# Performance work log

Measured on AMD Instinct MI355X. Metric: run time of the kernel, lower is better.

Reference implementation:

```python
import jax, jax.numpy as jnp
import numpy as np

B_, L, HID = 2, 1024, 2048
N, H, P, NA = 128, 64, 64, 32   # state, heads, head_dim, rope angle pairs
DIN = 2 * H * P + 2 * N + 3 * H + NA  # 8672
EPS = 1e-5
A_FLOOR = 1e-4


def setup_inputs() -> dict:
    key = jax.random.key(0)
    k0, k1, k2 = jax.random.split(key, 3)
    hidden_states = jax.random.normal(k0, (B_, L, HID), jnp.float32)
    in_proj_w = jax.random.normal(k1, (DIN, HID), jnp.float32) * 0.02
    out_proj_w = jax.random.normal(k2, (HID, H * P), jnp.float32) * 0.02
    # dt_bias init exactly as in the torch module
    rng = np.random.default_rng(0)
    dt = np.exp(rng.random(H) * (np.log(0.1) - np.log(0.001)) + np.log(0.001))
    dt = np.clip(dt, 1e-4, None)
    dt_bias = jnp.asarray(dt + np.log(-np.expm1(-dt)), jnp.float32)
    return {
        'hidden_states': hidden_states,
        'in_proj_w': in_proj_w,
        'dt_bias': dt_bias,
        'B_bias': jnp.ones((H, N), jnp.float32),
        'C_bias': jnp.ones((H, N), jnp.float32),
        'B_norm_w': jnp.ones((N,), jnp.float32),
        'C_norm_w': jnp.ones((N,), jnp.float32),
        'D': jnp.ones((H,), jnp.float32),
        'out_proj_w': out_proj_w,
    }


def _rmsnorm(x, w):
    var = jnp.mean(jnp.square(x), axis=-1, keepdims=True)
    return x * jax.lax.rsqrt(var + EPS) * w


def _forward(hidden_states, in_proj_w, dt_bias, B_bias, C_bias,
             B_norm_w, C_norm_w, D, out_proj_w):
    b, l, _ = hidden_states.shape
    proj = hidden_states @ in_proj_w.T  # (b,l,DIN)
    splits = np.cumsum([H * P, H * P, N, N, H, H, H])
    z, x, Braw, Craw, dd_dt, dd_A, trap, angles = jnp.split(proj, splits, axis=-1)
    z = z.reshape(b, l, H, P)
    x = x.reshape(b, l, H, P)
    # data-dependent A (per token, per head), clamped
    A = jnp.minimum(-jax.nn.softplus(dd_A.astype(jnp.float32)), -A_FLOOR)
    DT = jax.nn.softplus(dd_dt + dt_bias)          # (b,l,H)
    decay = jnp.exp(A * DT)                        # (b,l,H)
    lam = jax.nn.sigmoid(trap)                     # trapezoidal weight (b,l,H)
    # RMSNorm then per-head input-independent bias (n_groups=1, mimo_rank=1)
    Bn = _rmsnorm(Braw, B_norm_w)[:, :, None, :] + B_bias  # (b,l,H,N)
    Cn = _rmsnorm(Craw, C_norm_w)[:, :, None, :] + C_bias  # (b,l,H,N)
    # blockwise rotary on first 2*NA state dims, cumulative data-dependent phase
    phase = jnp.cumsum(angles[:, :, None, :].astype(jnp.float32) * DT[..., None], axis=1)  # (b,l,H,NA)
    cos, sin = jnp.cos(phase), jnp.sin(phase)

    def rope(v):
        v1, v2, rest = v[..., :NA], v[..., NA:2 * NA], v[..., 2 * NA:]
        return jnp.concatenate([v1 * cos - v2 * sin, v1 * sin + v2 * cos, rest], axis=-1)

    Bh = rope(Bn.astype(jnp.float32))
    Ch = rope(Cn.astype(jnp.float32))
    u = (x * DT[..., None]).astype(jnp.float32)    # (b,l,H,P)

    # selective scan with generalized trapezoidal discretization:
    # h_t = a_t h_{t-1} + (1-lam_t) u_t B_t^T + lam_t a_t u_{t-1} B_{t-1}^T
    def step(carry, inp):
        h, Gp = carry
        Bt, Ct, ut, dec, lm = inp
        G = ut[..., :, None] * Bt[..., None, :]    # (b,H,P,N)
        h = dec[..., None, None] * h + (1.0 - lm)[..., None, None] * G \
            + (lm * dec)[..., None, None] * Gp
        y = jnp.einsum('bhpn,bhn->bhp', h, Ct)
        return (h, G), y

    h0 = jnp.zeros((b, H, P, N), jnp.float32)
    xs = (Bh.transpose(1, 0, 2, 3), Ch.transpose(1, 0, 2, 3),
          u.transpose(1, 0, 2, 3), decay.transpose(1, 0, 2), lam.transpose(1, 0, 2))
    _, ys = jax.lax.scan(step, (h0, h0), xs)       # (l,b,H,P)
    y = ys.transpose(1, 0, 2, 3)
    y = y + D[None, None, :, None] * x             # skip connection
    y = y * jax.nn.silu(z)                         # output gate (Z path in kernel)
    y = y.reshape(b, l, H * P)
    return y @ out_proj_w.T


def reference(hidden_states, in_proj_w, dt_bias, B_bias, C_bias,
              B_norm_w, C_norm_w, D, out_proj_w):
    return _forward(hidden_states, in_proj_w, dt_bias, B_bias, C_bias,
                    B_norm_w, C_norm_w, D, out_proj_w)
```

## Files before the change

### kernel.cpp

```cpp
#include <hip/hip_runtime.h>
#include <hip/hip_bf16.h>
#include <cstdint>
#include <cstddef>

#define DEVINL __device__ __forceinline__

typedef __attribute__((ext_vector_type(8))) short bf16x8;
typedef __attribute__((ext_vector_type(4))) float f32x4;

DEVINL float bf2f(unsigned short u){
  union { unsigned u32; float f; } cv; cv.u32 = ((unsigned)u) << 16; return cv.f;
}
DEVINL unsigned short f2bf(float f){
  union { float f; unsigned u32; } cv; cv.f = f;
  unsigned u = cv.u32;
  return (unsigned short)((u + 0x7FFFu + ((u >> 16) & 1u)) >> 16);
}
DEVINL float softplusf(float x){ return x > 20.f ? x : log1pf(expf(x)); }

DEVINL void g2l16(const void* gptr, void* ldsptr){
  __builtin_amdgcn_global_load_lds(
      (const __attribute__((address_space(1))) unsigned int*)gptr,
      (__attribute__((address_space(3))) unsigned int*)(uintptr_t)ldsptr,
      16, 0, 0);
}

DEVINL int swzb(int row, int col){ return row*256 + ((col*2) ^ ((row&7)<<4)); }
DEVINL void ldsw_write8(unsigned short* b, int row, int col, bf16x8 v){
  *(bf16x8*)((char*)b + swzb(row,col)) = v;
}
DEVINL bf16x8 ldsw_read8(const unsigned short* b, int row, int col){
  return *(const bf16x8*)((const char*)b + swzb(row,col));
}
DEVINL void ldsw_write1(unsigned short* b, int row, int col, unsigned short v){
  *(unsigned short*)((char*)b + swzb(row,col)) = v;
}
DEVINL unsigned short ldsw_read1(const unsigned short* b, int row, int col){
  return *(const unsigned short*)((const char*)b + swzb(row,col));
}

__global__ __launch_bounds__(256) void k_f32_to_bf16(
    const float* __restrict__ in, unsigned short* __restrict__ out, long n)
{
  long i = ((long)blockIdx.x * 256 + threadIdx.x) * 4;
  if (i + 3 < n){
    float4 v = *(const float4*)(in + i);
    unsigned long long pk =
        (unsigned long long)f2bf(v.x)
      | ((unsigned long long)f2bf(v.y) << 16)
      | ((unsigned long long)f2bf(v.z) << 32)
      | ((unsigned long long)f2bf(v.w) << 48);
    *(unsigned long long*)(out + i) = pk;
  }
}

template<bool OUT_BF16>
__global__ __launch_bounds__(256) void k_gemm_bt(
    const unsigned short* __restrict__ A,
    const unsigned short* __restrict__ Bt,
    void* __restrict__ Cout,
    int K, int Nrows, int Npad, int tiles_n)
{
  __shared__ unsigned short Asub[128*64];
  __shared__ unsigned short Bsub[128*64];
  const int tid = threadIdx.x;
  const int nwg = gridDim.x;
  const int wg = ((nwg & 7) == 0) ? (int)((blockIdx.x & 7) * (nwg >> 3) + (blockIdx.x >> 3))
                                  : (int)blockIdx.x;
  const int rt = wg / tiles_n, ct = wg % tiles_n;
  const int lane = tid & 63, wave = tid >> 6;
  const int wr = wave >> 1, wc = wave & 1;
  const int fr = lane & 15;
  const int fq = lane >> 4;

  const int srow0 = tid >> 3;
  const int sgrp  = (tid & 7) ^ ((tid >> 3) & 7);
  size_t aoff[4], boff[4];
  #pragma unroll
  for (int i = 0; i < 4; i++){
    int row = i*32 + srow0;
    aoff[i] = (size_t)(rt*128 + row) * K + sgrp*8;
    int brow = ct*128 + row; if (brow > Nrows-1) brow = Nrows-1;
    boff[i] = (size_t)brow * K + sgrp*8;
  }

  f32x4 acc[4][4] = {};

  for (int k0 = 0; k0 < K; k0 += 64){
    #pragma unroll
    for (int i = 0; i < 4; i++){
      g2l16(A  + aoff[i] + k0, (char*)Asub + (i*256 + tid)*16);
      g2l16(Bt + boff[i] + k0, (char*)Bsub + (i*256 + tid)*16);
    }
    asm volatile("s_waitcnt vmcnt(0)" ::: "memory");
    __syncthreads();

    #pragma unroll
    for (int kk = 0; kk < 2; kk++){
      bf16x8 af[4], bfr[4];
      const int slot = (kk*4 + fq) ^ (fr & 7);
      #pragma unroll
      for (int i = 0; i < 4; i++){
        int ra = wr*64 + i*16 + fr;
        int rb = wc*64 + i*16 + fr;
        af[i]  = *(const bf16x8*)((const char*)Asub + ra*128 + slot*16);
        bfr[i] = *(const bf16x8*)((const char*)Bsub + rb*128 + slot*16);
      }
      #pragma unroll
      for (int mi = 0; mi < 4; mi++)
        #pragma unroll
        for (int ni = 0; ni < 4; ni++)
          acc[mi][ni] = __builtin_amdgcn_mfma_f32_16x16x32_bf16(af[mi], bfr[ni], acc[mi][ni], 0, 0, 0);
    }
    __syncthreads();
  }

  const int er = (lane >> 4) * 4;
  const int ec = lane & 15;
  #pragma unroll
  for (int mi = 0; mi < 4; mi++){
    #pragma unroll
    for (int ni = 0; ni < 4; ni++){
      const int row = rt*128 + wr*64 + mi*16 + er;
      const int col = ct*128 + wc*64 + ni*16 + ec;
      #pragma unroll
      for (int r = 0; r < 4; r++){
        if (OUT_BF16)
          ((unsigned short*)Cout)[(size_t)(row+r)*Npad + col] = f2bf(acc[mi][ni][r]);
        else
          ((float*)Cout)[(size_t)(row+r)*Npad + col] = acc[mi][ni][r];
      }
    }
  }
}

__global__ __launch_bounds__(256) void k_prep_scalars(
    const unsigned short* __restrict__ proj, const float* __restrict__ dt_bias,
    float* __restrict__ DTt, float* __restrict__ logdec, float* __restrict__ lamt)
{
  int idx = blockIdx.x*256 + threadIdx.x;
  int h = idx & 63, row = idx >> 6;
  int b = row >> 10, l = row & 1023;
  size_t base = (size_t)row * 8704;
  float dd_dt = bf2f(proj[base + 8448 + h]);
  float dd_A  = bf2f(proj[base + 8512 + h]);
  float trap  = bf2f(proj[base + 8576 + h]);
  float DT = softplusf(dd_dt + dt_bias[h]);
  float A  = -fmaxf(softplusf(dd_A), 1e-4f);
  size_t o = ((size_t)(b*64 + h))*1024 + l;
  DTt[o]    = DT;
  logdec[o] = A * DT;
  lamt[o]   = 1.f / (1.f + expf(-trap));
}

__global__ __launch_bounds__(128) void k_rmsnorm(
    const unsigned short* __restrict__ proj, const float* __restrict__ Bw,
    const float* __restrict__ Cw, unsigned short* __restrict__ Bb2,
    unsigned short* __restrict__ Cb2)
{
  int row = blockIdx.x, n = threadIdx.x;
  size_t base = (size_t)row * 8704;
  float bv = bf2f(proj[base + 8192 + n]);
  float cv = bf2f(proj[base + 8320 + n]);
  float sb = bv*bv, sc = cv*cv;
  #pragma unroll
  for (int m = 1; m < 64; m <<= 1){ sb += __shfl_xor(sb, m, 64); sc += __shfl_xor(sc, m, 64); }
  __shared__ float red[4];
  if ((n & 63) == 0){ red[(n>>6)*2] = sb; red[(n>>6)*2+1] = sc; }
  __syncthreads();
  sb = red[0] + red[2];
  sc = red[1] + red[3];
  float rb = rsqrtf(sb*(1.f/128.f) + 1e-5f);
  float rc = rsqrtf(sc*(1.f/128.f) + 1e-5f);
  Bb2[row*128 + n] = f2bf(bv*rb*Bw[n]);
  Cb2[row*128 + n] = f2bf(cv*rc*Cw[n]);
}

__global__ __launch_bounds__(256) void k_chunkscan(
    const float* __restrict__ logdec, const float* __restrict__ lamt,
    float* __restrict__ clcb, float* __restrict__ gb)
{
  int bh = blockIdx.x;
  size_t base = (size_t)bh * 1024;
  int tid = threadIdx.x;
  int e0 = tid * 4;
  float v0 = logdec[base+e0], v1 = logdec[base+e0+1], v2 = logdec[base+e0+2], v3 = logdec[base+e0+3];
  float p0 = v0, p1 = p0+v1, p2 = p1+v2, p3 = p2+v3;
  float tot = p3;
  int sub = tid & 31;
  float incl = tot;
  #pragma unroll
  for (int off = 1; off < 32; off <<= 1){
    float u = __shfl_up(incl, off, 32);
    if (sub >= off) incl += u;
  }
  float excl = incl - tot;
  clcb[base+e0]   = excl + p0;
  clcb[base+e0+1] = excl + p1;
  clcb[base+e0+2] = excl + p2;
  clcb[base+e0+3] = excl + p3;
  #pragma unroll
  for (int i = 0; i < 4; i++){
    int l = e0 + i;
    int ln = (l == 1023) ? 1023 : l + 1;
    gb[base+l] = 1.f - lamt[base+l] + lamt[base+ln];
  }
}

__global__ __launch_bounds__(256) void k_phase(
    const unsigned short* __restrict__ proj, const float* __restrict__ DTt,
    unsigned short* __restrict__ cosb, unsigned short* __restrict__ sinb)
{
  int bh = blockIdx.x, b = bh >> 6, h = bh & 63;
  int na = threadIdx.x & 31, c = threadIdx.x >> 5;
  __shared__ float part[8][32];
  const float* dtr = DTt + (size_t)bh * 1024;
  float s = 0.f;
  for (int i = 0; i < 128; i++){
    int l = c*128 + i; int row = b*1024 + l;
    float ang = bf2f(proj[(size_t)row*8704 + 8640 + na]);
    s = fmaf(ang, dtr[l], s);
  }
  part[c][na] = s;
  __syncthreads();
  float off = 0.f;
  for (int cc = 0; cc < c; cc++) off += part[cc][na];
  float ph = off;
  for (int i = 0; i < 128; i++){
    int l = c*128 + i; int row = b*1024 + l;
    float ang = bf2f(proj[(size_t)row*8704 + 8640 + na]);
    ph = fmaf(ang, dtr[l], ph);
    float sn, cs;
    __sincosf(ph, &sn, &cs);
    size_t o = ((size_t)row*64 + h)*32 + na;
    cosb[o] = f2bf(cs); sinb[o] = f2bf(sn);
  }
}

__global__ __launch_bounds__(256, 1) void k_intra(
    const unsigned short* __restrict__ proj,
    const unsigned short* __restrict__ Bb2, const unsigned short* __restrict__ Cb2,
    const float* __restrict__ Bbias, const float* __restrict__ Cbias,
    const unsigned short* __restrict__ cosb, const unsigned short* __restrict__ sinb,
    const float* __restrict__ DTt, const float* __restrict__ clcb,
    const float* __restrict__ gb, const float* __restrict__ lamt,
    const float* __restrict__ Dv, unsigned short* __restrict__ ybf,
    unsigned short* __restrict__ Gbuf)
{
  const int c = blockIdx.x & 7, bh = blockIdx.x >> 3;
  const int b = bh >> 6, h = bh & 63;
  const int tid = threadIdx.x, lane = tid & 63, wave = tid >> 6;
  const int wr = wave >> 1, wc = wave & 1;
  const int fr = lane & 15, fq = lane >> 4;

  __shared__ __align__(16) unsigned short Cs[128*128];
  __shared__ __align__(16) unsigned short Bs[128*128];
  __shared__ __align__(16) unsigned short BTs[128*128];
  __shared__ __align__(16) unsigned short Uts[64*128];
  __shared__ float clcs[128], lams[128], gs[128], wUs[128], dts[128];
  __shared__ float biasB[128], biasC[128];

  const int base = b*1024 + c*128;
  const size_t shbase = (size_t)bh * 1024;
  const float Dh = Dv[h];

  if (tid < 128){
    int l = c*128 + tid;
    clcs[tid] = clcb[shbase + l];
    dts[tid]  = DTt[shbase + l];
    lams[tid] = lamt[shbase + l];
    gs[tid]   = gb[shbase + l];
    biasB[tid] = Bbias[h*128 + tid];
  } else {
    biasC[tid-128] = Cbias[h*128 + tid-128];
  }
  __syncthreads();
  if (tid < 128) wUs[tid] = __expf(clcs[127] - clcs[tid]) * gs[tid];

  {
    const int t = tid >> 1, half = tid & 1;
    const int grow = base + t;
    const size_t roff = (size_t)grow*128 + half*64;
    if (half == 0){
      bf16x8 cc[4], sv[4];
      #pragma unroll
      for (int i = 0; i < 4; i++){
        cc[i] = *(const bf16x8*)(cosb + ((size_t)grow*64 + h)*32 + i*8);
        sv[i] = *(const bf16x8*)(sinb + ((size_t)grow*64 + h)*32 + i*8);
      }
      #pragma unroll
      for (int i = 0; i < 4; i++){
        bf16x8 vlo = *(const bf16x8*)(Cb2 + roff + i*8);
        bf16x8 vhi = *(const bf16x8*)(Cb2 + roff + 32 + i*8);
        bf16x8 olo, ohi;
        #pragma unroll
        for (int e = 0; e < 8; e++){
          float a = bf2f((unsigned short)vlo[e]) + biasC[i*8+e];
          float d = bf2f((unsigned short)vhi[e]) + biasC[32+i*8+e];
          float cf = bf2f((unsigned short)cc[i][e]);
          float sf = bf2f((unsigned short)sv[i][e]);
          olo[e] = (short)f2bf(a*cf - d*sf);
          ohi[e] = (short)f2bf(a*sf + d*cf);
        }
        ldsw_write8(Cs, t, i*8, olo);
        ldsw_write8(Cs, t, 32 + i*8, ohi);
      }
      #pragma unroll
      for (int i = 0; i < 4; i++){
        bf16x8 vlo = *(const bf16x8*)(Bb2 + roff + i*8);
        bf16x8 vhi = *(const bf16x8*)(Bb2 + roff + 32 + i*8);
        bf16x8 olo, ohi;
        #pragma unroll
        for (int e = 0; e < 8; e++){
          float a = bf2f((unsigned short)vlo[e]) + biasB[i*8+e];
          float d = bf2f((unsigned short)vhi[e]) + biasB[32+i*8+e];
          float cf = bf2f((unsigned short)cc[i][e]);
          float sf = bf2f((unsigned short)sv[i][e]);
          olo[e] = (short)f2bf(a*cf - d*sf);
          ohi[e] = (short)f2bf(a*sf + d*cf);
        }
        ldsw_write8(Bs, t, i*8, olo);
        ldsw_write8(Bs, t, 32 + i*8, ohi);
        #pragma unroll
        for (int e = 0; e < 8; e++){
          ldsw_write1(BTs, i*8+e, t, (unsigned short)olo[e]);
          ldsw_write1(BTs, 32+i*8+e, t, (unsigned short)ohi[e]);
        }
      }
    } else {
      #pragma unroll
      for (int i = 0; i < 8; i++){
        bf16x8 v = *(const bf16x8*)(Cb2 + roff + i*8);
        bf16x8 o;
        #pragma unroll
        for (int e = 0; e < 8; e++) o[e] = (short)f2bf(bf2f((unsigned short)v[e]) + biasC[64+i*8+e]);
        ldsw_write8(Cs, t, 64 + i*8, o);
      }
      #pragma unroll
      for (int i = 0; i < 8; i++){
        bf16x8 v = *(const bf16x8*)(Bb2 + roff + i*8);
        bf16x8 o;
        #pragma unroll
        for (int e = 0; e < 8; e++) o[e] = (short)f2bf(bf2f((unsigned short)v[e]) + biasB[64+i*8+e]);
        ldsw_write8(Bs, t, 64 + i*8, o);
        #pragma unroll
        for (int e = 0; e < 8; e++) ldsw_write1(BTs, 64+i*8+e, t, (unsigned short)o[e]);
      }
    }
  }
  {
    const int p = tid & 63, jg = tid >> 6;
    #pragma unroll 4
    for (int i = 0; i < 32; i++){
      int j = jg*32 + i;
      size_t pb = (size_t)(base + j) * 8704;
      float x  = bf2f(proj[pb + 4096 + h*64 + p]);
      ldsw_write1(Uts, p, j, f2bf(x * dts[j]));
    }
  }
  __syncthreads();

  f32x4 acc1[4][4];
  #pragma unroll
  for (int mi = 0; mi < 4; mi++)
    #pragma unroll
    for (int ni = 0; ni < 4; ni++)
      acc1[mi][ni] = (f32x4){0.f,0.f,0.f,0.f};
  #pragma unroll
  for (int ks = 0; ks < 4; ks++){
    bf16x8 af[4], bj[4];
    #pragma unroll
    for (int mi = 0; mi < 4; mi++) af[mi] = ldsw_read8(Cs, wr*64+mi*16+fr, ks*32+fq*8);
    #pragma unroll
    for (int ni = 0; ni < 4; ni++) bj[ni] = ldsw_read8(Bs, wc*64+ni*16+fr, ks*32+fq*8);
    #pragma unroll
    for (int mi = 0; mi < 4; mi++)
      #pragma unroll
      for (int ni = 0; ni < 4; ni++)
        acc1[mi][ni] = __builtin_amdgcn_mfma_f32_16x16x32_bf16(af[mi], bj[ni], acc1[mi][ni], 0,0,0);
  }
  unsigned short pr[4][4][4];
  int jj[4]; float clcj[4], gj[4];
  #pragma unroll
  for (int ni = 0; ni < 4; ni++){ jj[ni] = wc*64+ni*16+fr; clcj[ni] = clcs[jj[ni]]; gj[ni] = gs[jj[ni]]; }
  #pragma unroll
  for (int mi = 0; mi < 4; mi++){
    #pragma unroll
    for (int r = 0; r < 4; r++){
      int t = wr*64+mi*16+fq*4+r;
      float ct = clcs[t], lt = lams[t];
      #pragma unroll
      for (int ni = 0; ni < 4; ni++){
        int j = jj[ni];
        float w = (j < t) ? __expf(ct - clcj[ni])*gj[ni] : ((j == t) ? (1.f - lt) : 0.f);
        pr[mi][ni][r] = f2bf(acc1[mi][ni][r] * w);
      }
    }
  }
  __syncthreads();
  #pragma unroll
  for (int mi = 0; mi < 4; mi++)
    #pragma unroll
    for (int ni = 0; ni < 4; ni++)
      #pragma unroll
      for (int r = 0; r < 4; r++)
        ldsw_write1(Bs, wr*64+mi*16+fq*4+r, wc*64+ni*16+fr, pr[mi][ni][r]);
  __syncthreads();

  f32x4 acc2[4][2];
  #pragma unroll
  for (int mi = 0; mi < 4; mi++)
    #pragma unroll
    for (int ni = 0; ni < 2; ni++)
      acc2[mi][ni] = (f32x4){0.f,0.f,0.f,0.f};
  #pragma unroll
  for (int ks = 0; ks < 4; ks++){
    bf16x8 af[4], uj[2];
    #pragma unroll
    for (int mi = 0; mi < 4; mi++) af[mi] = ldsw_read8(Bs, wr*64+mi*16+fr, ks*32+fq*8);
    #pragma unroll
    for (int ni = 0; ni < 2; ni++) uj[ni] = ldsw_read8(Uts, wc*32+ni*16+fr, ks*32+fq*8);
    #pragma unroll
    for (int mi = 0; mi < 4; mi++)
      #pragma unroll
      for (int ni = 0; ni < 2; ni++)
        acc2[mi][ni] = __builtin_amdgcn_mfma_f32_16x16x32_bf16(af[mi], uj[ni], acc2[mi][ni], 0,0,0);
  }
  f32x4 accS[2][4];
  #pragma unroll
  for (int mi = 0; mi < 2; mi++)
    #pragma unroll
    for (int ni = 0; ni < 4; ni++)
      accS[mi][ni] = (f32x4){0.f,0.f,0.f,0.f};
  #pragma unroll
  for (int ks = 0; ks < 4; ks++){
    bf16x8 au[2], bn[4];
    #pragma unroll
    for (int mi = 0; mi < 2; mi++){
      bf16x8 raw = ldsw_read8(Uts, wr*32+mi*16+fr, ks*32+fq*8);
      #pragma unroll
      for (int e = 0; e < 8; e++){
        float f = bf2f((unsigned short)raw[e]) * wUs[ks*32+fq*8+e];
        au[mi][e] = (short)f2bf(f);
      }
    }
    #pragma unroll
    for (int ni = 0; ni < 4; ni++) bn[ni] = ldsw_read8(BTs, wc*64+ni*16+fr, ks*32+fq*8);
    #pragma unroll
    for (int mi = 0; mi < 2; mi++)
      #pragma unroll
      for (int ni = 0; ni < 4; ni++)
        accS[mi][ni] = __builtin_amdgcn_mfma_f32_16x16x32_bf16(au[mi], bn[ni], accS[mi][ni], 0,0,0);
  }

  #pragma unroll
  for (int mi = 0; mi < 4; mi++){
    #pragma unroll
    for (int ni = 0; ni < 2; ni++){
      #pragma unroll
      for (int r = 0; r < 4; r++){
        int t = wr*64+mi*16+fq*4+r;
        int p = wc*32+ni*16+fr;
        float xv = bf2f(ldsw_read1(Uts, p, t)) / fmaxf(dts[t], 1e-30f);
        float o = acc2[mi][ni][r] + Dh*xv;
        ybf[(size_t)(base + t)*4096 + h*64 + p] = f2bf(o);
      }
    }
  }
  #pragma unroll
  for (int mi = 0; mi < 2; mi++)
    #pragma unroll
    for (int ni = 0; ni < 4; ni++)
      #pragma unroll
      for (int r = 0; r < 4; r++){
        int p = wr*32+mi*16+fq*4+r;
        int n = wc*64+ni*16+fr;
        Gbuf[(size_t)blockIdx.x*8192 + p*128 + n] = f2bf(accS[mi][ni][r]);
      }
}

__global__ __launch_bounds__(256) void k_scanstate(
    const float* __restrict__ clcb, unsigned short* __restrict__ Gbuf)
{
  const int bh = blockIdx.x, tid = threadIdx.x;
  float S[32];
  #pragma unroll
  for (int i = 0; i < 32; i++) S[i] = 0.f;
  const size_t gbase = (size_t)bh*65536 + (size_t)tid*32;
  for (int c = 0; c < 8; c++){
    float decEnd = __expf(clcb[(size_t)bh*1024 + c*128 + 127]);
    unsigned short* p = Gbuf + gbase + (size_t)c*8192;
    bf16x8 g[4], s[4];
    #pragma unroll
    for (int i = 0; i < 4; i++) g[i] = *(const bf16x8*)(p + i*8);
    #pragma unroll
    for (int i = 0; i < 4; i++)
      #pragma unroll
      for (int e = 0; e < 8; e++) s[i][e] = (short)f2bf(S[i*8+e]);
    #pragma unroll
    for (int i = 0; i < 4; i++) *(bf16x8*)(p + i*8) = s[i];
    #pragma unroll
    for (int i = 0; i < 4; i++)
      #pragma unroll
      for (int e = 0; e < 8; e++)
        S[i*8+e] = decEnd*S[i*8+e] + bf2f((unsigned short)g[i][e]);
  }
}

__global__ __launch_bounds__(256) void k_inter(
    const unsigned short* __restrict__ proj,
    const unsigned short* __restrict__ Cb2, const float* __restrict__ Cbias,
    const unsigned short* __restrict__ cosb, const unsigned short* __restrict__ sinb,
    const float* __restrict__ clcb, const unsigned short* __restrict__ Sprev,
    unsigned short* __restrict__ ybf)
{
  const int c = blockIdx.x & 7, bh = blockIdx.x >> 3;
  const int b = bh >> 6, h = bh & 63;
  const int tid = threadIdx.x, lane = tid & 63, wave = tid >> 6;
  const int wr = wave >> 1, wc = wave & 1;
  const int fr = lane & 15, fq = lane >> 4;

  __shared__ __align__(16) unsigned short Cs[128*128];
  __shared__ __align__(16) unsigned short Ss[64*128];
  __shared__ float expclcs[128], biasC[128];

  const int base = b*1024 + c*128;

  if (tid < 128){
    expclcs[tid] = __expf(clcb[(size_t)bh*1024 + c*128 + tid]);
    biasC[tid] = Cbias[h*128 + tid];
  }
  __syncthreads();

  {
    const int t = tid >> 1, half = tid & 1;
    const int grow = base + t;
    const size_t roff = (size_t)grow*128 + half*64;
    if (half == 0){
      bf16x8 cc[4], sv[4];
      #pragma unroll
      for (int i = 0; i < 4; i++){
        cc[i] = *(const bf16x8*)(cosb + ((size_t)grow*64 + h)*32 + i*8);
        sv[i] = *(const bf16x8*)(sinb + ((size_t)grow*64 + h)*32 + i*8);
      }
      #pragma unroll
      for (int i = 0; i < 4; i++){
        bf16x8 vlo = *(const bf16x8*)(Cb2 + roff + i*8);
        bf16x8 vhi = *(const bf16x8*)(Cb2 + roff + 32 + i*8);
        bf16x8 olo, ohi;
        #pragma unroll
        for (int e = 0; e < 8; e++){
          float a = bf2f((unsigned short)vlo[e]) + biasC[i*8+e];
          float d = bf2f((unsigned short)vhi[e]) + biasC[32+i*8+e];
          float cf = bf2f((unsigned short)cc[i][e]);
          float sf = bf2f((unsigned short)sv[i][e]);
          olo[e] = (short)f2bf(a*cf - d*sf);
          ohi[e] = (short)f2bf(a*sf + d*cf);
        }
        ldsw_write8(Cs, t, i*8, olo);
        ldsw_write8(Cs, t, 32 + i*8, ohi);
      }
    } else {
      #pragma unroll
      for (int i = 0; i < 8; i++){
        bf16x8 v = *(const bf16x8*)(Cb2 + roff + i*8);
        bf16x8 o;
        #pragma unroll
        for (int e = 0; e < 8; e++) o[e] = (short)f2bf(bf2f((unsigned short)v[e]) + biasC[64+i*8+e]);
        ldsw_write8(Cs, t, 64 + i*8, o);
      }
    }
  }
  {
    const unsigned short* src = Sprev + (size_t)blockIdx.x*8192 + (size_t)tid*32;
    #pragma unroll
    for (int i = 0; i < 4; i++){
      bf16x8 v = *(const bf16x8*)(src + i*8);
      int f = tid*32 + i*8;
      ldsw_write8(Ss, f >> 7, f & 127, v);
    }
  }
  __syncthreads();

  f32x4 acc[4][2];
  #pragma unroll
  for (int mi = 0; mi < 4; mi++)
    #pragma unroll
    for (int ni = 0; ni < 2; ni++)
      acc[mi][ni] = (f32x4){0.f,0.f,0.f,0.f};
  #pragma unroll
  for (int ks = 0; ks < 4; ks++){
    bf16x8 af[4], sj[2];
    #pragma unroll
    for (int mi = 0; mi < 4; mi++) af[mi] = ldsw_read8(Cs, wr*64+mi*16+fr, ks*32+fq*8);
    #pragma unroll
    for (int ni = 0; ni < 2; ni++) sj[ni] = ldsw_read8(Ss, wc*32+ni*16+fr, ks*32+fq*8);
    #pragma unroll
    for (int mi = 0; mi < 4; mi++)
      #pragma unroll
      for (int ni = 0; ni < 2; ni++)
        acc[mi][ni] = __builtin_amdgcn_mfma_f32_16x16x32_bf16(af[mi], sj[ni], acc[mi][ni], 0,0,0);
  }

  #pragma unroll
  for (int mi = 0; mi < 4; mi++){
    #pragma unroll
    for (int ni = 0; ni < 2; ni++){
      #pragma unroll
      for (int r = 0; r < 4; r++){
        int t = wr*64+mi*16+fq*4+r;
        int p = wc*32+ni*16+fr;
        size_t yoff = (size_t)(base + t)*4096 + h*64 + p;
        float y = bf2f(ybf[yoff]) + expclcs[t]*acc[mi][ni][r];
        float zv = bf2f(proj[(size_t)(base + t)*8704 + h*64 + p]);
        float sl = zv / (1.f + __expf(-zv));
        ybf[yoff] = f2bf(y * sl);
      }
    }
  }
}

extern "C" void kernel_launch(void* const* d_in, const int* in_sizes, int n_in,
                              void* d_out, int out_size, void* d_ws, size_t ws_size,
                              hipStream_t stream)
{
  const float* hs    = (const float*)d_in[0];
  const float* w1    = (const float*)d_in[1];
  const float* dtb   = (const float*)d_in[2];
  const float* Bbias = (const float*)d_in[3];
  const float* Cbias = (const float*)d_in[4];
  const float* Bw    = (const float*)d_in[5];
  const float* Cw    = (const float*)d_in[6];
  const float* Dv    = (const float*)d_in[7];
  const float* wo    = (const float*)d_in[8];
  float* out = (float*)d_out;
  char* ws = (char*)d_ws;

  unsigned short* projbf = (unsigned short*)(ws + 0UL);
  unsigned short* W1bf   = (unsigned short*)(ws + 35651584UL);
  unsigned short* Gbuf   = W1bf;
  unsigned short* Wobf   = W1bf;
  unsigned short* ybf    = (unsigned short*)(ws + 52428800UL);
  unsigned short* hsbf   = (unsigned short*)(ws + 71172096UL);
  unsigned short* cosb   = hsbf;
  unsigned short* sinb   = (unsigned short*)(ws + 79560704UL);
  float* DTt    = (float*)(ws + 87949312UL);
  float* logdec = (float*)(ws + 88473600UL);
  float* lamt   = (float*)(ws + 88997888UL);
  float* clcb   = (float*)(ws + 89522176UL);
  float* gb     = (float*)(ws + 90046464UL);
  unsigned short* Bb2 = (unsigned short*)(ws + 90570752UL);
  unsigned short* Cb2 = (unsigned short*)(ws + 91095040UL);
  if (ws_size < 91619328UL) return;

  (void)in_sizes; (void)n_in; (void)out_size;

  k_f32_to_bf16<<<17344, 256, 0, stream>>>(w1, W1bf, 17760256L);
  k_f32_to_bf16<<<4096,  256, 0, stream>>>(hs, hsbf, 4194304L);
  k_gemm_bt<true><<<16*68, 256, 0, stream>>>(hsbf, W1bf, projbf, 2048, 8672, 8704, 68);
  k_prep_scalars<<<512, 256, 0, stream>>>(projbf, dtb, DTt, logdec, lamt);
  k_rmsnorm<<<2048, 128, 0, stream>>>(projbf, Bw, Cw, Bb2, Cb2);
  k_chunkscan<<<128, 256, 0, stream>>>(logdec, lamt, clcb, gb);
  k_phase<<<128, 256, 0, stream>>>(projbf, DTt, cosb, sinb);
  k_intra<<<1024, 256, 0, stream>>>(projbf, Bb2, Cb2, Bbias, Cbias,
                                    cosb, sinb, DTt, clcb, gb, lamt, Dv, ybf, Gbuf);
  k_scanstate<<<128, 256, 0, stream>>>(clcb, Gbuf);
  k_inter<<<1024, 256, 0, stream>>>(projbf, Cb2, Cbias, cosb, sinb, clcb, Gbuf, ybf);
  k_f32_to_bf16<<<8192, 256, 0, stream>>>(wo, Wobf, 8388608L);
  k_gemm_bt<false><<<16*16, 256, 0, stream>>>(ybf, Wobf, out, 4096, 2048, 2048, 16);
}
```

Baseline: 341.3 us.

## Use XCD-aware tile mapping in GEMMs and fuse small scalar kernels

The GEMM block-to-tile mapping now assigns each of the 8 XCDs (blockIdx & 7) a contiguous rectangular sub-grid of output tiles. The aim is to improve L2 reuse of A and B panels within each XCD. Separately, the per-token scalar prep is fused into the RMSNorm kernel and the chunk cumulative-sum is fused into the phase kernel, removing two launches and some extra passes over memory. The tile-mapping parameters must exactly cover the grid (2x8 rows by 4x17 cols for the first GEMM, 4x4 by 2x8 for the second), so a wrong set would silently skip or duplicate tiles.

```diff
diff --git a/kernel.cpp b/kernel.cpp
--- a/kernel.cpp
+++ b/kernel.cpp
@@ -59,15 +59,14 @@
     const unsigned short* __restrict__ A,
     const unsigned short* __restrict__ Bt,
     void* __restrict__ Cout,
-    int K, int Nrows, int Npad, int tiles_n)
+    int K, int Nrows, int Npad, int xm, int tmx, int tnx)
 {
   __shared__ unsigned short Asub[128*64];
   __shared__ unsigned short Bsub[128*64];
   const int tid = threadIdx.x;
-  const int nwg = gridDim.x;
-  const int wg = ((nwg & 7) == 0) ? (int)((blockIdx.x & 7) * (nwg >> 3) + (blockIdx.x >> 3))
-                                  : (int)blockIdx.x;
-  const int rt = wg / tiles_n, ct = wg % tiles_n;
+  const int x = blockIdx.x & 7, i = blockIdx.x >> 3;
+  const int rt = (x % xm) * tmx + (i % tmx);
+  const int ct = (x / xm) * tnx + (i / tmx);
   const int lane = tid & 63, wave = tid >> 6;
   const int wr = wave >> 1, wc = wave & 1;
   const int fr = lane & 15;
@@ -77,20 +76,20 @@
   const int sgrp  = (tid & 7) ^ ((tid >> 3) & 7);
   size_t aoff[4], boff[4];
   #pragma unroll
-  for (int i = 0; i < 4; i++){
-    int row = i*32 + srow0;
-    aoff[i] = (size_t)(rt*128 + row) * K + sgrp*8;
+  for (int j = 0; j < 4; j++){
+    int row = j*32 + srow0;
+    aoff[j] = (size_t)(rt*128 + row) * K + sgrp*8;
     int brow = ct*128 + row; if (brow > Nrows-1) brow = Nrows-1;
-    boff[i] = (size_t)brow * K + sgrp*8;
+    boff[j] = (size_t)brow * K + sgrp*8;
   }
 
   f32x4 acc[4][4] = {};
 
   for (int k0 = 0; k0 < K; k0 += 64){
     #pragma unroll
-    for (int i = 0; i < 4; i++){
-      g2l16(A  + aoff[i] + k0, (char*)Asub + (i*256 + tid)*16);
-      g2l16(Bt + boff[i] + k0, (char*)Bsub + (i*256 + tid)*16);
+    for (int j = 0; j < 4; j++){
+      g2l16(A  + aoff[j] + k0, (char*)Asub + (j*256 + tid)*16);
+      g2l16(Bt + boff[j] + k0, (char*)Bsub + (j*256 + tid)*16);
     }
     asm volatile("s_waitcnt vmcnt(0)" ::: "memory");
     __syncthreads();
@@ -100,11 +99,11 @@
       bf16x8 af[4], bfr[4];
       const int slot = (kk*4 + fq) ^ (fr & 7);
       #pragma unroll
-      for (int i = 0; i < 4; i++){
-        int ra = wr*64 + i*16 + fr;
-        int rb = wc*64 + i*16 + fr;
-        af[i]  = *(const bf16x8*)((const char*)Asub + ra*128 + slot*16);
-        bfr[i] = *(const bf16x8*)((const char*)Bsub + rb*128 + slot*16);
+      for (int j = 0; j < 4; j++){
+        int ra = wr*64 + j*16 + fr;
+        int rb = wc*64 + j*16 + fr;
+        af[j]  = *(const bf16x8*)((const char*)Asub + ra*128 + slot*16);
+        bfr[j] = *(const bf16x8*)((const char*)Bsub + rb*128 + slot*16);
       }
       #pragma unroll
       for (int mi = 0; mi < 4; mi++)
@@ -134,29 +133,11 @@
   }
 }
 
-__global__ __launch_bounds__(256) void k_prep_scalars(
-    const unsigned short* __restrict__ proj, const float* __restrict__ dt_bias,
+__global__ __launch_bounds__(128) void k_rmsprep(
+    const unsigned short* __restrict__ proj, const float* __restrict__ Bw,
+    const float* __restrict__ Cw, const float* __restrict__ dt_bias,
+    unsigned short* __restrict__ Bb2, unsigned short* __restrict__ Cb2,
     float* __restrict__ DTt, float* __restrict__ logdec, float* __restrict__ lamt)
-{
-  int idx = blockIdx.x*256 + threadIdx.x;
-  int h = idx & 63, row = idx >> 6;
-  int b = row >> 10, l = row & 1023;
-  size_t base = (size_t)row * 8704;
-  float dd_dt = bf2f(proj[base + 8448 + h]);
-  float dd_A  = bf2f(proj[base + 8512 + h]);
-  float trap  = bf2f(proj[base + 8576 + h]);
-  float DT = softplusf(dd_dt + dt_bias[h]);
-  float A  = -fmaxf(softplusf(dd_A), 1e-4f);
-  size_t o = ((size_t)(b*64 + h))*1024 + l;
-  DTt[o]    = DT;
-  logdec[o] = A * DT;
-  lamt[o]   = 1.f / (1.f + expf(-trap));
-}
-
-__global__ __launch_bounds__(128) void k_rmsnorm(
-    const unsigned short* __restrict__ proj, const float* __restrict__ Bw,
-    const float* __restrict__ Cw, unsigned short* __restrict__ Bb2,
-    unsigned short* __restrict__ Cb2)
 {
   int row = blockIdx.x, n = threadIdx.x;
   size_t base = (size_t)row * 8704;
@@ -174,50 +155,60 @@
   float rc = rsqrtf(sc*(1.f/128.f) + 1e-5f);
   Bb2[row*128 + n] = f2bf(bv*rb*Bw[n]);
   Cb2[row*128 + n] = f2bf(cv*rc*Cw[n]);
-}
-
-__global__ __launch_bounds__(256) void k_chunkscan(
-    const float* __restrict__ logdec, const float* __restrict__ lamt,
-    float* __restrict__ clcb, float* __restrict__ gb)
-{
-  int bh = blockIdx.x;
-  size_t base = (size_t)bh * 1024;
-  int tid = threadIdx.x;
-  int e0 = tid * 4;
-  float v0 = logdec[base+e0], v1 = logdec[base+e0+1], v2 = logdec[base+e0+2], v3 = logdec[base+e0+3];
-  float p0 = v0, p1 = p0+v1, p2 = p1+v2, p3 = p2+v3;
-  float tot = p3;
-  int sub = tid & 31;
-  float incl = tot;
-  #pragma unroll
-  for (int off = 1; off < 32; off <<= 1){
-    float u = __shfl_up(incl, off, 32);
-    if (sub >= off) incl += u;
-  }
-  float excl = incl - tot;
-  clcb[base+e0]   = excl + p0;
-  clcb[base+e0+1] = excl + p1;
-  clcb[base+e0+2] = excl + p2;
-  clcb[base+e0+3] = excl + p3;
-  #pragma unroll
-  for (int i = 0; i < 4; i++){
-    int l = e0 + i;
-    int ln = (l == 1023) ? 1023 : l + 1;
-    gb[base+l] = 1.f - lamt[base+l] + lamt[base+ln];
+  if (n < 64){
+    int h = n, b = row >> 10, l = row & 1023;
+    float dd_dt = bf2f(proj[base + 8448 + h]);
+    float dd_A  = bf2f(proj[base + 8512 + h]);
+    float trap  = bf2f(proj[base + 8576 + h]);
+    float DT = softplusf(dd_dt + dt_bias[h]);
+    float A  = -fmaxf(softplusf(dd_A), 1e-4f);
+    size_t o = ((size_t)(b*64 + h))*1024 + l;
+    DTt[o]    = DT;
+    logdec[o] = A * DT;
+    lamt[o]   = 1.f / (1.f + expf(-trap));
   }
 }
 
 __global__ __launch_bounds__(256) void k_phase(
     const unsigned short* __restrict__ proj, const float* __restrict__ DTt,
+    const float* __restrict__ logdec, const float* __restrict__ lamt,
+    float* __restrict__ clcb, float* __restrict__ gb,
     unsigned short* __restrict__ cosb, unsigned short* __restrict__ sinb)
 {
   int bh = blockIdx.x, b = bh >> 6, h = bh & 63;
-  int na = threadIdx.x & 31, c = threadIdx.x >> 5;
+  int tid = threadIdx.x;
+  size_t sbase = (size_t)bh * 1024;
+  {
+    int e0 = tid * 4;
+    float v0 = logdec[sbase+e0], v1 = logdec[sbase+e0+1],
+          v2 = logdec[sbase+e0+2], v3 = logdec[sbase+e0+3];
+    float p0 = v0, p1 = p0+v1, p2 = p1+v2, p3 = p2+v3;
+    float tot = p3;
+    int sub = tid & 31;
+    float incl = tot;
+    #pragma unroll
+    for (int off = 1; off < 32; off <<= 1){
+      float u = __shfl_up(incl, off, 32);
+      if (sub >= off) incl += u;
+    }
+    float excl = incl - tot;
+    clcb[sbase+e0]   = excl + p0;
+    clcb[sbase+e0+1] = excl + p1;
+    clcb[sbase+e0+2] = excl + p2;
+    clcb[sbase+e0+3] = excl + p3;
+    #pragma unroll
+    for (int q = 0; q < 4; q++){
+      int l = e0 + q;
+      int ln = (l == 1023) ? 1023 : l + 1;
+      gb[sbase+l] = 1.f - lamt[sbase+l] + lamt[sbase+ln];
+    }
+  }
+  int na = tid & 31, c = tid >> 5;
   __shared__ float part[8][32];
-  const float* dtr = DTt + (size_t)bh * 1024;
+  const float* dtr = DTt + sbase;
   float s = 0.f;
-  for (int i = 0; i < 128; i++){
-    int l = c*128 + i; int row = b*1024 + l;
+  for (int q = 0; q < 128; q++){
+    int l = c*128 + q; int row = b*1024 + l;
     float ang = bf2f(proj[(size_t)row*8704 + 8640 + na]);
     s = fmaf(ang, dtr[l], s);
   }
@@ -226,8 +217,8 @@
   float off = 0.f;
   for (int cc = 0; cc < c; cc++) off += part[cc][na];
   float ph = off;
-  for (int i = 0; i < 128; i++){
-    int l = c*128 + i; int row = b*1024 + l;
+  for (int q = 0; q < 128; q++){
+    int l = c*128 + q; int row = b*1024 + l;
     float ang = bf2f(proj[(size_t)row*8704 + 8640 + na]);
     ph = fmaf(ang, dtr[l], ph);
     float sn, cs;
@@ -284,78 +275,78 @@
     if (half == 0){
       bf16x8 cc[4], sv[4];
       #pragma unroll
-      for (int i = 0; i < 4; i++){
-        cc[i] = *(const bf16x8*)(cosb + ((size_t)grow*64 + h)*32 + i*8);
-        sv[i] = *(const bf16x8*)(sinb + ((size_t)grow*64 + h)*32 + i*8);
-      }
-      #pragma unroll
-      for (int i = 0; i < 4; i++){
-        bf16x8 vlo = *(const bf16x8*)(Cb2 + roff + i*8);
-        bf16x8 vhi = *(const bf16x8*)(Cb2 + roff + 32 + i*8);
+      for (int j = 0; j < 4; j++){
+        cc[j] = *(const bf16x8*)(cosb + ((size_t)grow*64 + h)*32 + j*8);
+        sv[j] = *(const bf16x8*)(sinb + ((size_t)grow*64 + h)*32 + j*8);
+      }
+      #pragma unroll
+      for (int j = 0; j < 4; j++){
+        bf16x8 vlo = *(const bf16x8*)(Cb2 + roff + j*8);
+        bf16x8 vhi = *(const bf16x8*)(Cb2 + roff + 32 + j*8);
         bf16x8 olo, ohi;
         #pragma unroll
         for (int e = 0; e < 8; e++){
-          float a = bf2f((unsigned short)vlo[e]) + biasC[i*8+e];
-          float d = bf2f((unsigned short)vhi[e]) + biasC[32+i*8+e];
-          float cf = bf2f((unsigned short)cc[i][e]);
-          float sf = bf2f((unsigned short)sv[i][e]);
+          float a = bf2f((unsigned short)vlo[e]) + biasC[j*8+e];
+          float d = bf2f((unsigned short)vhi[e]) + biasC[32+j*8+e];
+          float cf = bf2f((unsigned short)cc[j][e]);
+          float sf = bf2f((unsigned short)sv[j][e]);
           olo[e] = (short)f2bf(a*cf - d*sf);
           ohi[e] = (short)f2bf(a*sf + d*cf);
         }
-        ldsw_write8(Cs, t, i*8, olo);
-        ldsw_write8(Cs, t, 32 + i*8, ohi);
-      }
-      #pragma unroll
-      for (int i = 0; i < 4; i++){
-        bf16x8 vlo = *(const bf16x8*)(Bb2 + roff + i*8);
-        bf16x8 vhi = *(const bf16x8*)(Bb2 + roff + 32 + i*8);
+        ldsw_write8(Cs, t, j*8, olo);
+        ldsw_write8(Cs, t, 32 + j*8, ohi);
+      }
+      #pragma unroll
+      for (int j = 0; j < 4; j++){
+        bf16x8 vlo = *(const bf16x8*)(Bb2 + roff + j*8);
+        bf16x8 vhi = *(const bf16x8*)(Bb2 + roff + 32 + j*8);
         bf16x8 olo, ohi;
         #pragma unroll
         for (int e = 0; e < 8; e++){
-          float a = bf2f((unsigned short)vlo[e]) + biasB[i*8+e];
-          float d = bf2f((unsigned short)vhi[e]) + biasB[32+i*8+e];
-          float cf = bf2f((unsigned short)cc[i][e]);
-          float sf = bf2f((unsigned short)sv[i][e]);
+          float a = bf2f((unsigned short)vlo[e]) + biasB[j*8+e];
+          float d = bf2f((unsigned short)vhi[e]) + biasB[32+j*8+e];
+          float cf = bf2f((unsigned short)cc[j][e]);
+          float sf = bf2f((unsigned short)sv[j][e]);
           olo[e] = (short)f2bf(a*cf - d*sf);
           ohi[e] = (short)f2bf(a*sf + d*cf);
         }
-        ldsw_write8(Bs, t, i*8, olo);
-        ldsw_write8(Bs, t, 32 + i*8, ohi);
+        ldsw_write8(Bs, t, j*8, olo);
+        ldsw_write8(Bs, t, 32 + j*8, ohi);
         #pragma unroll
         for (int e = 0; e < 8; e++){
-          ldsw_write1(BTs, i*8+e, t, (unsigned short)olo[e]);
-          ldsw_write1(BTs, 32+i*8+e, t, (unsigned short)ohi[e]);
+          ldsw_write1(BTs, j*8+e, t, (unsigned short)olo[e]);
+          ldsw_write1(BTs, 32+j*8+e, t, (unsigned short)ohi[e]);
         }
       }
     } else {
       #pragma unroll
-      for (int i = 0; i < 8; i++){
-        bf16x8 v = *(const bf16x8*)(Cb2 + roff + i*8);
+      for (int j = 0; j < 8; j++){
+        bf16x8 v = *(const bf16x8*)(Cb2 + roff + j*8);
         bf16x8 o;
         #pragma unroll
-        for (int e = 0; e < 8; e++) o[e] = (short)f2bf(bf2f((unsigned short)v[e]) + biasC[64+i*8+e]);
-        ldsw_write8(Cs, t, 64 + i*8, o);
-      }
-      #pragma unroll
-      for (int i = 0; i < 8; i++){
-        bf16x8 v = *(const bf16x8*)(Bb2 + roff + i*8);
+        for (int e = 0; e < 8; e++) o[e] = (short)f2bf(bf2f((unsigned short)v[e]) + biasC[64+j*8+e]);
+        ldsw_write8(Cs, t, 64 + j*8, o);
+      }
+      #pragma unroll
+      for (int j = 0; j < 8; j++){
+        bf16x8 v = *(const bf16x8*)(Bb2 + roff + j*8);
         bf16x8 o;
         #pragma unroll
-        for (int e = 0; e < 8; e++) o[e] = (short)f2bf(bf2f((unsigned short)v[e]) + biasB[64+i*8+e]);
-        ldsw_write8(Bs, t, 64 + i*8, o);
-        #pragma unroll
-        for (int e = 0; e < 8; e++) ldsw_write1(BTs, 64+i*8+e, t, (unsigned short)o[e]);
+        for (int e = 0; e < 8; e++) o[e] = (short)f2bf(bf2f((unsigned short)v[e]) + biasB[64+j*8+e]);
+        ldsw_write8(Bs, t, 64 + j*8, o);
+        #pragma unroll
+        for (int e = 0; e < 8; e++) ldsw_write1(BTs, 64+j*8+e, t, (unsigned short)o[e]);
       }
     }
   }
   {
     const int p = tid & 63, jg = tid >> 6;
     #pragma unroll 4
-    for (int i = 0; i < 32; i++){
-      int j = jg*32 + i;
+    for (int q = 0; q < 32; q++){
+      int j = jg*32 + q;
       size_t pb = (size_t)(base + j) * 8704;
-      float x  = bf2f(proj[pb + 4096 + h*64 + p]);
-      ldsw_write1(Uts, p, j, f2bf(x * dts[j]));
+      float xx = bf2f(proj[pb + 4096 + h*64 + p]);
+      ldsw_write1(Uts, p, j, f2bf(xx * dts[j]));
     }
   }
   __syncthreads();
@@ -388,11 +379,11 @@
     #pragma unroll
     for (int r = 0; r < 4; r++){
       int t = wr*64+mi*16+fq*4+r;
-      float ct = clcs[t], lt = lams[t];
+      float ct_ = clcs[t], lt = lams[t];
       #pragma unroll
       for (int ni = 0; ni < 4; ni++){
         int j = jj[ni];
-        float w = (j < t) ? __expf(ct - clcj[ni])*gj[ni] : ((j == t) ? (1.f - lt) : 0.f);
+        float w = (j < t) ? __expf(ct_ - clcj[ni])*gj[ni] : ((j == t) ? (1.f - lt) : 0.f);
         pr[mi][ni][r] = f2bf(acc1[mi][ni][r] * w);
       }
     }
@@ -485,25 +476,25 @@
   const int bh = blockIdx.x, tid = threadIdx.x;
   float S[32];
   #pragma unroll
-  for (int i = 0; i < 32; i++) S[i] = 0.f;
+  for (int q = 0; q < 32; q++) S[q] = 0.f;
   const size_t gbase = (size_t)bh*65536 + (size_t)tid*32;
   for (int c = 0; c < 8; c++){
     float decEnd = __expf(clcb[(size_t)bh*1024 + c*128 + 127]);
     unsigned short* p = Gbuf + gbase + (size_t)c*8192;
     bf16x8 g[4], s[4];
     #pragma unroll
-    for (int i = 0; i < 4; i++) g[i] = *(const bf16x8*)(p + i*8);
-    #pragma unroll
-    for (int i = 0; i < 4; i++)
-      #pragma unroll
-      for (int e = 0; e < 8; e++) s[i][e] = (short)f2bf(S[i*8+e]);
-    #pragma unroll
-    for (int i = 0; i < 4; i++) *(bf16x8*)(p + i*8) = s[i];
-    #pragma unroll
-    for (int i = 0; i < 4; i++)
+    for (int q = 0; q < 4; q++) g[q] = *(const bf16x8*)(p + q*8);
+    #pragma unroll
+    for (int q = 0; q < 4; q++)
+      #pragma unroll
+      for (int e = 0; e < 8; e++) s[q][e] = (short)f2bf(S[q*8+e]);
+    #pragma unroll
+    for (int q = 0; q < 4; q++) *(bf16x8*)(p + q*8) = s[q];
+    #pragma unroll
+    for (int q = 0; q < 4; q++)
       #pragma unroll
       for (int e = 0; e < 8; e++)
-        S[i*8+e] = decEnd*S[i*8+e] + bf2f((unsigned short)g[i][e]);
+        S[q*8+e] = decEnd*S[q*8+e] + bf2f((unsigned short)g[q][e]);
   }
 }
 
@@ -539,44 +530,44 @@
     if (half == 0){
       bf16x8 cc[4], sv[4];
       #pragma unroll
-      for (int i = 0; i < 4; i++){
-        cc[i] = *(const bf16x8*)(cosb + ((size_t)grow*64 + h)*32 + i*8);
-        sv[i] = *(const bf16x8*)(sinb + ((size_t)grow*64 + h)*32 + i*8);
-      }
-      #pragma unroll
-      for (int i = 0; i < 4; i++){
-        bf16x8 vlo = *(const bf16x8*)(Cb2 + roff + i*8);
-        bf16x8 vhi = *(const bf16x8*)(Cb2 + roff + 32 + i*8);
+      for (int j = 0; j < 4; j++){
+        cc[j] = *(const bf16x8*)(cosb + ((size_t)grow*64 + h)*32 + j*8);
+        sv[j] = *(const bf16x8*)(sinb + ((size_t)grow*64 + h)*32 + j*8);
+      }
+      #pragma unroll
+      for (int j = 0; j < 4; j++){
+        bf16x8 vlo = *(const bf16x8*)(Cb2 + roff + j*8);
+        bf16x8 vhi = *(const bf16x8*)(Cb2 + roff + 32 + j*8);
         bf16x8 olo, ohi;
         #pragma unroll
         for (int e = 0; e < 8; e++){
-          float a = bf2f((unsigned short)vlo[e]) + biasC[i*8+e];
-          float d = bf2f((unsigned short)vhi[e]) + biasC[32+i*8+e];
-          float cf = bf2f((unsigned short)cc[i][e]);
-          float sf = bf2f((unsigned short)sv[i][e]);
+          float a = bf2f((unsigned short)vlo[e]) + biasC[j*8+e];
+          float d = bf2f((unsigned short)vhi[e]) + biasC[32+j*8+e];
+          float cf = bf2f((unsigned short)cc[j][e]);
+          float sf = bf2f((unsigned short)sv[j][e]);
           olo[e] = (short)f2bf(a*cf - d*sf);
           ohi[e] = (short)f2bf(a*sf + d*cf);
         }
-        ldsw_write8(Cs, t, i*8, olo);
-        ldsw_write8(Cs, t, 32 + i*8, ohi);
+        ldsw_write8(Cs, t, j*8, olo);
+        ldsw_write8(Cs, t, 32 + j*8, ohi);
       }
     } else {
       #pragma unroll
-      for (int i = 0; i < 8; i++){
-        bf16x8 v = *(const bf16x8*)(Cb2 + roff + i*8);
+      for (int j = 0; j < 8; j++){
+        bf16x8 v = *(const bf16x8*)(Cb2 + roff + j*8);
         bf16x8 o;
         #pragma unroll
-        for (int e = 0; e < 8; e++) o[e] = (short)f2bf(bf2f((unsigned short)v[e]) + biasC[64+i*8+e]);
-        ldsw_write8(Cs, t, 64 + i*8, o);
+        for (int e = 0; e < 8; e++) o[e] = (short)f2bf(bf2f((unsigned short)v[e]) + biasC[64+j*8+e]);
+        ldsw_write8(Cs, t, 64 + j*8, o);
       }
     }
   }
   {
     const unsigned short* src = Sprev + (size_t)blockIdx.x*8192 + (size_t)tid*32;
     #pragma unroll
-    for (int i = 0; i < 4; i++){
-      bf16x8 v = *(const bf16x8*)(src + i*8);
-      int f = tid*32 + i*8;
+    for (int j = 0; j < 4; j++){
+      bf16x8 v = *(const bf16x8*)(src + j*8);
+      int f = tid*32 + j*8;
       ldsw_write8(Ss, f >> 7, f & 127, v);
     }
   }
@@ -657,15 +648,13 @@
 
   k_f32_to_bf16<<<17344, 256, 0, stream>>>(w1, W1bf, 17760256L);
   k_f32_to_bf16<<<4096,  256, 0, stream>>>(hs, hsbf, 4194304L);
-  k_gemm_bt<true><<<16*68, 256, 0, stream>>>(hsbf, W1bf, projbf, 2048, 8672, 8704, 68);
-  k_prep_scalars<<<512, 256, 0, stream>>>(projbf, dtb, DTt, logdec, lamt);
-  k_rmsnorm<<<2048, 128, 0, stream>>>(projbf, Bw, Cw, Bb2, Cb2);
-  k_chunkscan<<<128, 256, 0, stream>>>(logdec, lamt, clcb, gb);
-  k_phase<<<128, 256, 0, stream>>>(projbf, DTt, cosb, sinb);
+  k_gemm_bt<true><<<1088, 256, 0, stream>>>(hsbf, W1bf, projbf, 2048, 8672, 8704, 2, 8, 17);
+  k_rmsprep<<<2048, 128, 0, stream>>>(projbf, Bw, Cw, dtb, Bb2, Cb2, DTt, logdec, lamt);
+  k_phase<<<128, 256, 0, stream>>>(projbf, DTt, logdec, lamt, clcb, gb, cosb, sinb);
   k_intra<<<1024, 256, 0, stream>>>(projbf, Bb2, Cb2, Bbias, Cbias,
                                     cosb, sinb, DTt, clcb, gb, lamt, Dv, ybf, Gbuf);
   k_scanstate<<<128, 256, 0, stream>>>(clcb, Gbuf);
   k_inter<<<1024, 256, 0, stream>>>(projbf, Cb2, Cbias, cosb, sinb, clcb, Gbuf, ybf);
   k_f32_to_bf16<<<8192, 256, 0, stream>>>(wo, Wobf, 8388608L);
-  k_gemm_bt<false><<<16*16, 256, 0, stream>>>(ybf, Wobf, out, 4096, 2048, 2048, 16);
-}
+  k_gemm_bt<false><<<256, 256, 0, stream>>>(ybf, Wobf, out, 4096, 2048, 2048, 4, 4, 8);
+}
```

Result: faster. 331.3 us (-2.9%).
